# Kernel tuning notes

Measured on AMD Instinct MI355X. Metric: run time of the kernel, lower is better.

The kernel has to match this reference:

```python
import jax, jax.numpy as jnp
import numpy as np

B, N, L, H, N_NODE, STEP = 1024, 64, 64, 128, 50000, 2


def setup_inputs() -> dict:
    key = jax.random.key(0)
    ks = jax.random.split(key, 24)
    stdv = 1.0 / np.sqrt(H)
    u = lambda k, shape: jax.random.uniform(k, shape, jnp.float32, -stdv, stdv)
    emb = u(ks[0], (N_NODE + 1, H))
    emb = emb.at[0].set(0.0)  # padding_idx=0
    return {
        "A": jax.random.uniform(ks[1], (B, N, 2 * N), jnp.float32),
        "items": jax.random.randint(ks[2], (B, N), 0, N_NODE + 1, jnp.int32),
        "mask": jnp.ones((B, L), jnp.int32),
        "alias_input": jax.random.randint(ks[3], (B, L), 0, N, jnp.int32),
        "emb": emb,
        "w_in": u(ks[4], (H, H)), "b_in": u(ks[5], (H,)),
        "w_out": u(ks[6], (H, H)), "b_out": u(ks[7], (H,)),
        "b_iah": u(ks[8], (H,)), "b_oah": u(ks[9], (H,)),
        "wi": u(ks[10], (3 * H, 2 * H)), "bi": u(ks[11], (3 * H,)),
        "wh": u(ks[12], (3 * H, H)), "bh": u(ks[13], (3 * H,)),
        "w1": u(ks[14], (H, H)), "b1": u(ks[15], (H,)),
        "w2": u(ks[16], (H, H)), "b2": u(ks[17], (H,)),
        "wq": u(ks[18], (1, H)),
        "w3": u(ks[19], (H, 2 * H)), "b3": u(ks[20], (2 * H,))[:H],
    }


def _gru_cell(A, hidden, p):
    n = A.shape[1]
    h_in = hidden @ p["w_in"].T + p["b_in"]
    h_out = hidden @ p["w_out"].T + p["b_out"]
    input_in = jnp.einsum("bnm,bmh->bnh", A[:, :, :n], h_in) + p["b_iah"]
    input_out = jnp.einsum("bnm,bmh->bnh", A[:, :, n:], h_out) + p["b_oah"]
    input_emb = jnp.concatenate([input_in, input_out], axis=2)  # [B,N,2H]
    gi = input_emb @ p["wi"].T + p["bi"]
    gh = hidden @ p["wh"].T + p["bh"]
    i_r, i_i, i_n = jnp.split(gi, 3, axis=2)
    h_r, h_i, h_n = jnp.split(gh, 3, axis=2)
    update_gate = jax.nn.sigmoid(i_i + h_i)
    reset_gate = jax.nn.sigmoid(i_r + h_r)
    new_gate = jnp.tanh(reset_gate * h_n + i_n)
    return (1.0 - update_gate) * hidden + update_gate * new_gate


def reference(A, items, mask, alias_input, emb, w_in, b_in, w_out, b_out,
              b_iah, b_oah, wi, bi, wh, bh, w1, b1, w2, b2, wq, w3, b3):
    p = dict(w_in=w_in, b_in=b_in, w_out=w_out, b_out=b_out, b_iah=b_iah,
             b_oah=b_oah, wi=wi, bi=bi, wh=wh, bh=bh)
    hidden = emb[items]  # [B,N,H]
    for _ in range(STEP):
        hidden = _gru_cell(A, hidden, p)
    # gather session order: seq_hidden[b, l] = hidden[b, alias_input[b, l]]
    seq_hidden = jnp.take_along_axis(hidden, alias_input[:, :, None], axis=1)  # [B,L,H]
    last = jnp.sum(mask, axis=1) - 1  # [B]
    local_emb = jnp.take_along_axis(seq_hidden, last[:, None, None], axis=1)[:, 0]  # [B,H]
    q1 = (local_emb @ w1.T + b1)[:, None, :]
    q2 = seq_hidden @ w2.T + b2
    alpha = jax.nn.sigmoid(q1 + q2) @ wq.T  # [B,L,1]
    global_emb = jnp.sum(alpha * seq_hidden * mask[:, :, None].astype(seq_hidden.dtype), axis=1)
    return jnp.concatenate([local_emb, global_emb], axis=1) @ w3.T + b3
```

## Files before the change

kernel.cpp:

```cpp
#include <hip/hip_runtime.h>
#include <stdint.h>


#define BDIM 256
#define NB   1024
#define NN   64
#define HH   128
#define SH_STR 136
#define SX_STR 264

#define OFS_WIN  0
#define OFS_WOUT 16384
#define OFS_WI   32768
#define OFS_WH   131072
#define OFS_W2   180224
#define N_FRAGS  24576

typedef short v8s __attribute__((ext_vector_type(8)));
typedef float v4f __attribute__((ext_vector_type(4)));

__device__ __forceinline__ float b2f_lo(uint32_t u){
  union { uint32_t u; float f; } v; v.u = u << 16; return v.f;
}
__device__ __forceinline__ float b2f_hi(uint32_t u){
  union { uint32_t u; float f; } v; v.u = u & 0xffff0000u; return v.f;
}
__device__ __forceinline__ uint16_t f2b(float f){
  union { float f; uint32_t u; } v; v.f = f;
  uint32_t r = v.u + 0x7fffu + ((v.u >> 16) & 1u);
  return (uint16_t)(r >> 16);
}
__device__ __forceinline__ float b2f(uint16_t s){
  union { uint32_t u; float f; } v; v.u = ((uint32_t)s) << 16; return v.f;
}
__device__ __forceinline__ float sig_f(float x){ return 1.0f / (1.0f + __expf(-x)); }
__device__ __forceinline__ float tanh_f(float x){ return 1.0f - 2.0f / (__expf(2.0f*x) + 1.0f); }

__device__ __forceinline__ uint32_t pack2bf(float a, float b){
  union { float f; uint32_t u; } ua, ub; ua.f = a; ub.f = b;
  return __builtin_amdgcn_perm(ub.u + 0x8000u, ua.u + 0x8000u, 0x07060302u);
}

__device__ __forceinline__ v8s pack8(const float* __restrict__ p){
  float4 f0 = *reinterpret_cast<const float4*>(p);
  float4 f1 = *reinterpret_cast<const float4*>(p + 4);
  union { uint32_t u[4]; v8s v; } o;
  o.u[0] = pack2bf(f0.x, f0.y);
  o.u[1] = pack2bf(f0.z, f0.w);
  o.u[2] = pack2bf(f1.x, f1.y);
  o.u[3] = pack2bf(f1.z, f1.w);
  return o.v;
}

__device__ __forceinline__ v8s ldsA(const uint16_t* buf, int stride,
                                    int row_base, int k_base, int r, int q){
  return *reinterpret_cast<const v8s*>(&buf[(row_base + r) * stride + k_base + q * 8]);
}

__device__ __forceinline__ v8s ldfrag(const uint16_t* __restrict__ ws,
                                      int base, int tile, int lane){
  return *reinterpret_cast<const v8s*>(ws + base + (((size_t)tile * 64 + lane) << 3));
}

#define MFMA(a, b, c) __builtin_amdgcn_mfma_f32_16x16x32_bf16((a), (b), (c), 0, 0, 0)

__global__ __launch_bounds__(256) void pack_weights(
    const float* __restrict__ w_in, const float* __restrict__ w_out,
    const float* __restrict__ wi,   const float* __restrict__ wh,
    const float* __restrict__ w2,   uint16_t* __restrict__ ws)
{
  int gid = blockIdx.x * blockDim.x + threadIdx.x;
  if (gid >= N_FRAGS) return;
  const float* W; int C; int fi; int base;
  if (gid < 2048)       { W = w_in;  C = 128; fi = gid;         base = OFS_WIN; }
  else if (gid < 4096)  { W = w_out; C = 128; fi = gid - 2048;  base = OFS_WOUT; }
  else if (gid < 16384) { W = wi;    C = 256; fi = gid - 4096;  base = OFS_WI; }
  else if (gid < 22528) { W = wh;    C = 128; fi = gid - 16384; base = OFS_WH; }
  else                  { W = w2;    C = 128; fi = gid - 22528; base = OFS_W2; }
  int lane = fi & 63;
  int tile = fi >> 6;
  int tc   = C >> 5;
  int tr   = tile / tc, kc = tile - tr * tc;
  int r = lane & 15, q = lane >> 4;
  const float* p = W + (size_t)(tr * 16 + r) * C + kc * 32 + q * 8;
  *reinterpret_cast<v8s*>(ws + base + ((size_t)fi << 3)) = pack8(p);
}

__global__ __launch_bounds__(BDIM, 3) void srgnn_kernel(
    const float* __restrict__ A,
    const int*   __restrict__ items,
    const int*   __restrict__ mask,
    const int*   __restrict__ alias_input,
    const float* __restrict__ emb,
    const float* __restrict__ b_in,  const float* __restrict__ b_out,
    const float* __restrict__ b_iah, const float* __restrict__ b_oah,
    const float* __restrict__ bi,    const float* __restrict__ bh,
    const float* __restrict__ w1,    const float* __restrict__ b1,
    const float* __restrict__ b2,
    const float* __restrict__ wq,
    const float* __restrict__ w3,    const float* __restrict__ b3,
    const uint16_t* __restrict__ ws,
    float* __restrict__ out)
{
  __shared__ __align__(16) uint16_t sH[NN * SH_STR];
  __shared__ __align__(16) uint16_t sX[NN * SX_STR];
  __shared__ float sQ1[128], sGlob[128], sAPart[4][64], sAlpha[64];
  __shared__ int   sAliasRow[64], sMaskArr[64];

  const int t    = threadIdx.x;
  const int b    = blockIdx.x;
  const int lane = t & 63;
  const int wv   = __builtin_amdgcn_readfirstlane(t >> 6);
  const int r    = lane & 15;
  const int q    = lane >> 4;

  {
    const int* itb = items + b * NN;
    for (int j = t; j < NN * HH; j += BDIM) {
      int n = j >> 7, k = j & 127;
      sH[n * SH_STR + k] = f2b(emb[(size_t)itb[n] * HH + k]);
    }
    if (t < 64) {
      sAliasRow[t] = alias_input[b * 64 + t];
      sMaskArr[t]  = mask[b * 64 + t];
    }
  }

  v8s a2[4][2];
  {
    const int half = wv >> 1;
    #pragma unroll
    for (int mt = 0; mt < 4; ++mt)
      #pragma unroll
      for (int kk = 0; kk < 2; ++kk)
        a2[mt][kk] = pack8(A + (size_t)(b * NN + mt * 16 + r) * (2 * NN)
                             + half * 64 + kk * 32 + q * 8);
  }
  __syncthreads();

  for (int step = 0; step < 2; ++step) {
    {
      v8s a[4][4];
      #pragma unroll
      for (int mt = 0; mt < 4; ++mt)
        #pragma unroll
        for (int kk = 0; kk < 4; ++kk)
          a[mt][kk] = ldsA(sH, SH_STR, mt * 16, kk * 32, r, q);

      const int    wbase = (wv < 2) ? OFS_WIN : OFS_WOUT;
      const float* bsel  = (wv < 2) ? b_in : b_out;
      const int    ntofs = (wv < 2) ? 0 : 8;
      #pragma unroll 2
      for (int i = 0; i < 4; ++i) {
        int nt = wv * 4 + i;
        int tr = nt - ntofs;
        int c  = nt * 16 + r;
        float bini = bsel[tr * 16 + r];
        v4f acc0 = {bini, bini, bini, bini}, acc1 = acc0, acc2 = acc0, acc3 = acc0;
        #pragma unroll
        for (int kk = 0; kk < 4; ++kk) {
          v8s bf = ldfrag(ws, wbase, tr * 4 + kk, lane);
          acc0 = MFMA(a[0][kk], bf, acc0);
          acc1 = MFMA(a[1][kk], bf, acc1);
          acc2 = MFMA(a[2][kk], bf, acc2);
          acc3 = MFMA(a[3][kk], bf, acc3);
        }
        #pragma unroll
        for (int reg = 0; reg < 4; ++reg) {
          sX[(0  + q * 4 + reg) * SX_STR + c] = f2b(acc0[reg]);
          sX[(16 + q * 4 + reg) * SX_STR + c] = f2b(acc1[reg]);
          sX[(32 + q * 4 + reg) * SX_STR + c] = f2b(acc2[reg]);
          sX[(48 + q * 4 + reg) * SX_STR + c] = f2b(acc3[reg]);
        }
      }
    }

    {
      const float* bsel2 = (wv < 2) ? b_iah : b_oah;
      const int    wofs2 = (wv < 2) ? 0 : 128;
      #pragma unroll 1
      for (int i = 0; i < 4; ++i) {
        int nt = wv * 4 + i;
        int c  = nt * 16 + r;
        v8s b0, b1f;
        #pragma unroll
        for (int j = 0; j < 8; ++j) {
          b0[j]  = (short)sX[(q * 8 + j) * SX_STR + c];
          b1f[j] = (short)sX[(32 + q * 8 + j) * SX_STR + c];
        }
        float bini = bsel2[c - wofs2];
        v4f acc0 = {bini, bini, bini, bini}, acc1 = acc0, acc2 = acc0, acc3 = acc0;
        acc0 = MFMA(a2[0][0], b0, acc0); acc0 = MFMA(a2[0][1], b1f, acc0);
        acc1 = MFMA(a2[1][0], b0, acc1); acc1 = MFMA(a2[1][1], b1f, acc1);
        acc2 = MFMA(a2[2][0], b0, acc2); acc2 = MFMA(a2[2][1], b1f, acc2);
        acc3 = MFMA(a2[3][0], b0, acc3); acc3 = MFMA(a2[3][1], b1f, acc3);
        #pragma unroll
        for (int reg = 0; reg < 4; ++reg) {
          sX[(0  + q * 4 + reg) * SX_STR + c] = f2b(acc0[reg]);
          sX[(16 + q * 4 + reg) * SX_STR + c] = f2b(acc1[reg]);
          sX[(32 + q * 4 + reg) * SX_STR + c] = f2b(acc2[reg]);
          sX[(48 + q * 4 + reg) * SX_STR + c] = f2b(acc3[reg]);
        }
      }
    }
    __syncthreads();

    {
      const int h0 = wv * 32;
      uint32_t nhpk[2][8];

      #pragma unroll 1
      for (int u = 0; u < 2; ++u) {
        int h = h0 + u * 16 + r;
        float vR  = bi[h] + bh[h];
        float vI  = bi[128 + h] + bh[128 + h];
        float vNi = bi[256 + h];
        float vNh = bh[256 + h];
        v4f aR[4], aI[4], aNi[4], aNh[4];
        #pragma unroll
        for (int mt = 0; mt < 4; ++mt) {
          aR[mt]  = (v4f){vR, vR, vR, vR};
          aI[mt]  = (v4f){vI, vI, vI, vI};
          aNi[mt] = (v4f){vNi, vNi, vNi, vNi};
          aNh[mt] = (v4f){vNh, vNh, vNh, vNh};
        }
        const int trb = wv * 2 + u;
        #pragma unroll 2
        for (int kk = 0; kk < 8; ++kk) {
          v8s af0 = ldsA(sX, SX_STR, 0,  kk * 32, r, q);
          v8s af1 = ldsA(sX, SX_STR, 16, kk * 32, r, q);
          v8s af2 = ldsA(sX, SX_STR, 32, kk * 32, r, q);
          v8s af3 = ldsA(sX, SX_STR, 48, kk * 32, r, q);
          v8s bR = ldfrag(ws, OFS_WI, (0 * 8 + trb) * 8 + kk, lane);
          v8s bI = ldfrag(ws, OFS_WI, (8 + trb) * 8 + kk, lane);
          v8s bN = ldfrag(ws, OFS_WI, (16 + trb) * 8 + kk, lane);
          aR[0]  = MFMA(af0, bR, aR[0]);  aR[1]  = MFMA(af1, bR, aR[1]);
          aR[2]  = MFMA(af2, bR, aR[2]);  aR[3]  = MFMA(af3, bR, aR[3]);
          aI[0]  = MFMA(af0, bI, aI[0]);  aI[1]  = MFMA(af1, bI, aI[1]);
          aI[2]  = MFMA(af2, bI, aI[2]);  aI[3]  = MFMA(af3, bI, aI[3]);
          aNi[0] = MFMA(af0, bN, aNi[0]); aNi[1] = MFMA(af1, bN, aNi[1]);
          aNi[2] = MFMA(af2, bN, aNi[2]); aNi[3] = MFMA(af3, bN, aNi[3]);
        }
        #pragma unroll 2
        for (int kk = 0; kk < 4; ++kk) {
          v8s af0 = ldsA(sH, SH_STR, 0,  kk * 32, r, q);
          v8s af1 = ldsA(sH, SH_STR, 16, kk * 32, r, q);
          v8s af2 = ldsA(sH, SH_STR, 32, kk * 32, r, q);
          v8s af3 = ldsA(sH, SH_STR, 48, kk * 32, r, q);
          v8s bR = ldfrag(ws, OFS_WH, (0 * 8 + trb) * 4 + kk, lane);
          v8s bI = ldfrag(ws, OFS_WH, (8 + trb) * 4 + kk, lane);
          v8s bN = ldfrag(ws, OFS_WH, (16 + trb) * 4 + kk, lane);
          aR[0]  = MFMA(af0, bR, aR[0]);  aR[1]  = MFMA(af1, bR, aR[1]);
          aR[2]  = MFMA(af2, bR, aR[2]);  aR[3]  = MFMA(af3, bR, aR[3]);
          aI[0]  = MFMA(af0, bI, aI[0]);  aI[1]  = MFMA(af1, bI, aI[1]);
          aI[2]  = MFMA(af2, bI, aI[2]);  aI[3]  = MFMA(af3, bI, aI[3]);
          aNh[0] = MFMA(af0, bN, aNh[0]); aNh[1] = MFMA(af1, bN, aNh[1]);
          aNh[2] = MFMA(af2, bN, aNh[2]); aNh[3] = MFMA(af3, bN, aNh[3]);
        }
        #pragma unroll
        for (int mt = 0; mt < 4; ++mt) {
          #pragma unroll
          for (int rp = 0; rp < 2; ++rp) {
            uint32_t pk = 0;
            #pragma unroll
            for (int e = 0; e < 2; ++e) {
              int reg = rp * 2 + e;
              int row = mt * 16 + q * 4 + reg;
              float z  = sig_f(aI[mt][reg]);
              float rr = sig_f(aR[mt][reg]);
              float gg = tanh_f(fmaf(rr, aNh[mt][reg], aNi[mt][reg]));
              float hp = b2f(sH[row * SH_STR + h]);
              pk |= (uint32_t)f2b(fmaf(z, gg - hp, hp)) << (16 * e);
            }
            nhpk[u][mt * 2 + rp] = pk;
          }
        }
      }
      __syncthreads();

      #pragma unroll
      for (int u = 0; u < 2; ++u) {
        int h = h0 + u * 16 + r;
        #pragma unroll
        for (int mt = 0; mt < 4; ++mt)
          #pragma unroll
          for (int rp = 0; rp < 2; ++rp) {
            uint32_t pk = nhpk[u][mt * 2 + rp];
            int row = mt * 16 + q * 4 + rp * 2;
            sH[row * SH_STR + h]       = (uint16_t)(pk & 0xffff);
            sH[(row + 1) * SH_STR + h] = (uint16_t)(pk >> 16);
          }
      }
    }
    __syncthreads();
  }

  int msum = 0;
  #pragma unroll
  for (int l = 0; l < 64; ++l) msum += sMaskArr[l];
  const int lastRow = sAliasRow[msum - 1];

  if (t < HH) {
    const float4* w14 = reinterpret_cast<const float4*>(w1 + (size_t)t * HH);
    const uint2*  lr  = reinterpret_cast<const uint2*>(&sH[lastRow * SH_STR]);
    float a0 = b1[t], a1 = 0.f, a2v = 0.f, a3 = 0.f;
    #pragma unroll 8
    for (int j = 0; j < 32; ++j) {
      float4 w = w14[j]; uint2 v = lr[j];
      a0  = fmaf(b2f_lo(v.x), w.x, a0);  a1 = fmaf(b2f_hi(v.x), w.y, a1);
      a2v = fmaf(b2f_lo(v.y), w.z, a2v); a3 = fmaf(b2f_hi(v.y), w.w, a3);
    }
    sQ1[t] = (a0 + a1) + (a2v + a3);
  }
  __syncthreads();

  {
    v8s a[4][4];
    #pragma unroll
    for (int mt = 0; mt < 4; ++mt) {
      int row = sAliasRow[mt * 16 + r];
      #pragma unroll
      for (int kk = 0; kk < 4; ++kk)
        a[mt][kk] = *reinterpret_cast<const v8s*>(&sH[row * SH_STR + kk * 32 + q * 8]);
    }
    float part[16];
    #pragma unroll
    for (int i = 0; i < 16; ++i) part[i] = 0.f;
    #pragma unroll
    for (int u = 0; u < 2; ++u) {
      int h = wv * 32 + u * 16 + r;
      float binit = sQ1[h] + b2[h];
      v4f acc[4];
      #pragma unroll
      for (int mt = 0; mt < 4; ++mt) acc[mt] = (v4f){binit, binit, binit, binit};
      #pragma unroll
      for (int kk = 0; kk < 4; ++kk) {
        v8s bf = ldfrag(ws, OFS_W2, (wv * 2 + u) * 4 + kk, lane);
        acc[0] = MFMA(a[0][kk], bf, acc[0]);
        acc[1] = MFMA(a[1][kk], bf, acc[1]);
        acc[2] = MFMA(a[2][kk], bf, acc[2]);
        acc[3] = MFMA(a[3][kk], bf, acc[3]);
      }
      float wqh = wq[h];
      #pragma unroll
      for (int mt = 0; mt < 4; ++mt)
        #pragma unroll
        for (int reg = 0; reg < 4; ++reg)
          part[mt * 4 + reg] += sig_f(acc[mt][reg]) * wqh;
    }
    #pragma unroll
    for (int m = 1; m <= 8; m <<= 1)
      #pragma unroll
      for (int i = 0; i < 16; ++i)
        part[i] += __shfl_xor(part[i], m);
    if (r == 0) {
      #pragma unroll
      for (int mt = 0; mt < 4; ++mt)
        #pragma unroll
        for (int reg = 0; reg < 4; ++reg)
          sAPart[wv][mt * 16 + q * 4 + reg] = part[mt * 4 + reg];
    }
  }
  __syncthreads();
  if (t < 64) {
    sAlpha[t] = (sAPart[0][t] + sAPart[1][t] + sAPart[2][t] + sAPart[3][t])
              * (float)sMaskArr[t];
  }
  __syncthreads();
  if (t < HH) {
    float acc = 0.0f;
    #pragma unroll
    for (int l = 0; l < 64; ++l)
      acc = fmaf(sAlpha[l], b2f(sH[sAliasRow[l] * SH_STR + t]), acc);
    sGlob[t] = acc;
  }
  __syncthreads();
  if (t < HH) {
    const float4* w34 = reinterpret_cast<const float4*>(w3 + (size_t)t * 256);
    const uint2*  lr  = reinterpret_cast<const uint2*>(&sH[lastRow * SH_STR]);
    float a0 = b3[t], a1 = 0.f, a2v = 0.f, a3 = 0.f;
    #pragma unroll 8
    for (int j = 0; j < 32; ++j) {
      float4 w = w34[j]; uint2 v = lr[j];
      a0  = fmaf(b2f_lo(v.x), w.x, a0);  a1 = fmaf(b2f_hi(v.x), w.y, a1);
      a2v = fmaf(b2f_lo(v.y), w.z, a2v); a3 = fmaf(b2f_hi(v.y), w.w, a3);
    }
    const float4* w34b = w34 + 32;
    #pragma unroll 8
    for (int j = 0; j < 32; ++j) {
      float4 w = w34b[j];
      a0  = fmaf(sGlob[4*j+0], w.x, a0);  a1 = fmaf(sGlob[4*j+1], w.y, a1);
      a2v = fmaf(sGlob[4*j+2], w.z, a2v); a3 = fmaf(sGlob[4*j+3], w.w, a3);
    }
    out[b * HH + t] = (a0 + a1) + (a2v + a3);
  }
}

extern "C" void kernel_launch(void* const* d_in, const int* in_sizes, int n_in,
                              void* d_out, int out_size, void* d_ws, size_t ws_size,
                              hipStream_t stream) {
  const float* A          = (const float*)d_in[0];
  const int*   items      = (const int*)  d_in[1];
  const int*   mask       = (const int*)  d_in[2];
  const int*   alias_in   = (const int*)  d_in[3];
  const float* emb        = (const float*)d_in[4];
  const float* w_in       = (const float*)d_in[5];
  const float* b_in       = (const float*)d_in[6];
  const float* w_out      = (const float*)d_in[7];
  const float* b_out      = (const float*)d_in[8];
  const float* b_iah      = (const float*)d_in[9];
  const float* b_oah      = (const float*)d_in[10];
  const float* wi         = (const float*)d_in[11];
  const float* bi         = (const float*)d_in[12];
  const float* wh         = (const float*)d_in[13];
  const float* bh         = (const float*)d_in[14];
  const float* w1         = (const float*)d_in[15];
  const float* b1         = (const float*)d_in[16];
  const float* w2         = (const float*)d_in[17];
  const float* b2         = (const float*)d_in[18];
  const float* wq         = (const float*)d_in[19];
  const float* w3         = (const float*)d_in[20];
  const float* b3         = (const float*)d_in[21];
  float* out = (float*)d_out;
  uint16_t* wsp = (uint16_t*)d_ws;

  hipLaunchKernelGGL(pack_weights, dim3((N_FRAGS + 255) / 256), dim3(256), 0, stream,
                     w_in, w_out, wi, wh, w2, wsp);
  hipLaunchKernelGGL(srgnn_kernel, dim3(NB), dim3(BDIM), 0, stream,
                     A, items, mask, alias_in, emb,
                     b_in, b_out, b_iah, b_oah, bi, bh,
                     w1, b1, b2, wq, w3, b3, wsp, out);
}
```

Before: 257.5 us.

## Interleave GRU input/hidden MFMA loops, prefetch weight fragments, split epilogue across all threads

```diff
diff --git a/kernel.cpp b/kernel.cpp
--- a/kernel.cpp
+++ b/kernel.cpp
@@ -104,8 +104,14 @@
 {
   __shared__ __align__(16) uint16_t sH[NN * SH_STR];
   __shared__ __align__(16) uint16_t sX[NN * SX_STR];
-  __shared__ float sQ1[128], sGlob[128], sAPart[4][64], sAlpha[64];
-  __shared__ int   sAliasRow[64], sMaskArr[64];
+  __shared__ int sAliasRow[64], sMaskArr[64];
+
+  float* sF      = reinterpret_cast<float*>(sX);
+  float* sQ1v    = sF;
+  float* sGlobv  = sF + 128;
+  float* sAPartv = sF + 256;
+  float* sAlphav = sF + 512;
+  float* sP      = sF + 576;
 
   const int t    = threadIdx.x;
   const int b    = blockIdx.x;
@@ -203,6 +209,15 @@
         }
       }
     }
+
+    v8s pR[2], pI[2], pN[2];
+    #pragma unroll
+    for (int u = 0; u < 2; ++u) {
+      int trb = wv * 2 + u;
+      pR[u] = ldfrag(ws, OFS_WI, (0  + trb) * 8, lane);
+      pI[u] = ldfrag(ws, OFS_WI, (8  + trb) * 8, lane);
+      pN[u] = ldfrag(ws, OFS_WI, (16 + trb) * 8, lane);
+    }
     __syncthreads();
 
     {
@@ -225,37 +240,51 @@
           aNh[mt] = (v4f){vNh, vNh, vNh, vNh};
         }
         const int trb = wv * 2 + u;
-        #pragma unroll 2
-        for (int kk = 0; kk < 8; ++kk) {
+
+        #pragma unroll 1
+        for (int kk = 0; kk < 4; ++kk) {
+          v8s bR = (kk == 0) ? pR[u] : ldfrag(ws, OFS_WI, (0  + trb) * 8 + kk, lane);
+          v8s bI = (kk == 0) ? pI[u] : ldfrag(ws, OFS_WI, (8  + trb) * 8 + kk, lane);
+          v8s bN = (kk == 0) ? pN[u] : ldfrag(ws, OFS_WI, (16 + trb) * 8 + kk, lane);
+          v8s cR = ldfrag(ws, OFS_WH, (0  + trb) * 4 + kk, lane);
+          v8s cI = ldfrag(ws, OFS_WH, (8  + trb) * 4 + kk, lane);
+          v8s cN = ldfrag(ws, OFS_WH, (16 + trb) * 4 + kk, lane);
           v8s af0 = ldsA(sX, SX_STR, 0,  kk * 32, r, q);
           v8s af1 = ldsA(sX, SX_STR, 16, kk * 32, r, q);
           v8s af2 = ldsA(sX, SX_STR, 32, kk * 32, r, q);
           v8s af3 = ldsA(sX, SX_STR, 48, kk * 32, r, q);
-          v8s bR = ldfrag(ws, OFS_WI, (0 * 8 + trb) * 8 + kk, lane);
-          v8s bI = ldfrag(ws, OFS_WI, (8 + trb) * 8 + kk, lane);
-          v8s bN = ldfrag(ws, OFS_WI, (16 + trb) * 8 + kk, lane);
+          v8s ag0 = ldsA(sH, SH_STR, 0,  kk * 32, r, q);
+          v8s ag1 = ldsA(sH, SH_STR, 16, kk * 32, r, q);
+          v8s ag2 = ldsA(sH, SH_STR, 32, kk * 32, r, q);
+          v8s ag3 = ldsA(sH, SH_STR, 48, kk * 32, r, q);
           aR[0]  = MFMA(af0, bR, aR[0]);  aR[1]  = MFMA(af1, bR, aR[1]);
           aR[2]  = MFMA(af2, bR, aR[2]);  aR[3]  = MFMA(af3, bR, aR[3]);
           aI[0]  = MFMA(af0, bI, aI[0]);  aI[1]  = MFMA(af1, bI, aI[1]);
           aI[2]  = MFMA(af2, bI, aI[2]);  aI[3]  = MFMA(af3, bI, aI[3]);
           aNi[0] = MFMA(af0, bN, aNi[0]); aNi[1] = MFMA(af1, bN, aNi[1]);
           aNi[2] = MFMA(af2, bN, aNi[2]); aNi[3] = MFMA(af3, bN, aNi[3]);
+          aR[0]  = MFMA(ag0, cR, aR[0]);  aR[1]  = MFMA(ag1, cR, aR[1]);
+          aR[2]  = MFMA(ag2, cR, aR[2]);  aR[3]  = MFMA(ag3, cR, aR[3]);
+          aI[0]  = MFMA(ag0, cI, aI[0]);  aI[1]  = MFMA(ag1, cI, aI[1]);
+          aI[2]  = MFMA(ag2, cI, aI[2]);  aI[3]  = MFMA(ag3, cI, aI[3]);
+          aNh[0] = MFMA(ag0, cN, aNh[0]); aNh[1] = MFMA(ag1, cN, aNh[1]);
+          aNh[2] = MFMA(ag2, cN, aNh[2]); aNh[3] = MFMA(ag3, cN, aNh[3]);
         }
         #pragma unroll 2
-        for (int kk = 0; kk < 4; ++kk) {
-          v8s af0 = ldsA(sH, SH_STR, 0,  kk * 32, r, q);
-          v8s af1 = ldsA(sH, SH_STR, 16, kk * 32, r, q);
-          v8s af2 = ldsA(sH, SH_STR, 32, kk * 32, r, q);
-          v8s af3 = ldsA(sH, SH_STR, 48, kk * 32, r, q);
-          v8s bR = ldfrag(ws, OFS_WH, (0 * 8 + trb) * 4 + kk, lane);
-          v8s bI = ldfrag(ws, OFS_WH, (8 + trb) * 4 + kk, lane);
-          v8s bN = ldfrag(ws, OFS_WH, (16 + trb) * 4 + kk, lane);
+        for (int kk = 4; kk < 8; ++kk) {
+          v8s bR = ldfrag(ws, OFS_WI, (0  + trb) * 8 + kk, lane);
+          v8s bI = ldfrag(ws, OFS_WI, (8  + trb) * 8 + kk, lane);
+          v8s bN = ldfrag(ws, OFS_WI, (16 + trb) * 8 + kk, lane);
+          v8s af0 = ldsA(sX, SX_STR, 0,  kk * 32, r, q);
+          v8s af1 = ldsA(sX, SX_STR, 16, kk * 32, r, q);
+          v8s af2 = ldsA(sX, SX_STR, 32, kk * 32, r, q);
+          v8s af3 = ldsA(sX, SX_STR, 48, kk * 32, r, q);
           aR[0]  = MFMA(af0, bR, aR[0]);  aR[1]  = MFMA(af1, bR, aR[1]);
           aR[2]  = MFMA(af2, bR, aR[2]);  aR[3]  = MFMA(af3, bR, aR[3]);
           aI[0]  = MFMA(af0, bI, aI[0]);  aI[1]  = MFMA(af1, bI, aI[1]);
           aI[2]  = MFMA(af2, bI, aI[2]);  aI[3]  = MFMA(af3, bI, aI[3]);
-          aNh[0] = MFMA(af0, bN, aNh[0]); aNh[1] = MFMA(af1, bN, aNh[1]);
-          aNh[2] = MFMA(af2, bN, aNh[2]); aNh[3] = MFMA(af3, bN, aNh[3]);
+          aNi[0] = MFMA(af0, bN, aNi[0]); aNi[1] = MFMA(af1, bN, aNi[1]);
+          aNi[2] = MFMA(af2, bN, aNi[2]); aNi[3] = MFMA(af3, bN, aNi[3]);
         }
         #pragma unroll
         for (int mt = 0; mt < 4; ++mt) {
@@ -299,19 +328,23 @@
   #pragma unroll
   for (int l = 0; l < 64; ++l) msum += sMaskArr[l];
   const int lastRow = sAliasRow[msum - 1];
-
-  if (t < HH) {
-    const float4* w14 = reinterpret_cast<const float4*>(w1 + (size_t)t * HH);
-    const uint2*  lr  = reinterpret_cast<const uint2*>(&sH[lastRow * SH_STR]);
-    float a0 = b1[t], a1 = 0.f, a2v = 0.f, a3 = 0.f;
+  const int hh  = t & 127;
+  const int seg = t >> 7;
+
+  {
+    const float4* w14 = reinterpret_cast<const float4*>(w1 + (size_t)hh * HH + seg * 64);
+    const uint2*  lr  = reinterpret_cast<const uint2*>(&sH[lastRow * SH_STR + seg * 64]);
+    float a0 = seg ? 0.f : b1[hh], a1 = 0.f, a2v = 0.f, a3 = 0.f;
     #pragma unroll 8
-    for (int j = 0; j < 32; ++j) {
+    for (int j = 0; j < 16; ++j) {
       float4 w = w14[j]; uint2 v = lr[j];
       a0  = fmaf(b2f_lo(v.x), w.x, a0);  a1 = fmaf(b2f_hi(v.x), w.y, a1);
       a2v = fmaf(b2f_lo(v.y), w.z, a2v); a3 = fmaf(b2f_hi(v.y), w.w, a3);
     }
-    sQ1[t] = (a0 + a1) + (a2v + a3);
-  }
+    sP[seg * 128 + hh] = (a0 + a1) + (a2v + a3);
+  }
+  __syncthreads();
+  if (t < HH) sQ1v[t] = sP[t] + sP[128 + t];
   __syncthreads();
 
   {
@@ -329,7 +362,7 @@
     #pragma unroll
     for (int u = 0; u < 2; ++u) {
       int h = wv * 32 + u * 16 + r;
-      float binit = sQ1[h] + b2[h];
+      float binit = sQ1v[h] + b2[h];
       v4f acc[4];
       #pragma unroll
       for (int mt = 0; mt < 4; ++mt) acc[mt] = (v4f){binit, binit, binit, binit};
@@ -358,42 +391,52 @@
       for (int mt = 0; mt < 4; ++mt)
         #pragma unroll
         for (int reg = 0; reg < 4; ++reg)
-          sAPart[wv][mt * 16 + q * 4 + reg] = part[mt * 4 + reg];
+          sAPartv[wv * 64 + mt * 16 + q * 4 + reg] = part[mt * 4 + reg];
     }
   }
   __syncthreads();
   if (t < 64) {
-    sAlpha[t] = (sAPart[0][t] + sAPart[1][t] + sAPart[2][t] + sAPart[3][t])
-              * (float)sMaskArr[t];
-  }
-  __syncthreads();
-  if (t < HH) {
+    sAlphav[t] = (sAPartv[t] + sAPartv[64 + t] + sAPartv[128 + t] + sAPartv[192 + t])
+               * (float)sMaskArr[t];
+  }
+  __syncthreads();
+
+  {
     float acc = 0.0f;
     #pragma unroll
-    for (int l = 0; l < 64; ++l)
-      acc = fmaf(sAlpha[l], b2f(sH[sAliasRow[l] * SH_STR + t]), acc);
-    sGlob[t] = acc;
-  }
-  __syncthreads();
-  if (t < HH) {
-    const float4* w34 = reinterpret_cast<const float4*>(w3 + (size_t)t * 256);
-    const uint2*  lr  = reinterpret_cast<const uint2*>(&sH[lastRow * SH_STR]);
-    float a0 = b3[t], a1 = 0.f, a2v = 0.f, a3 = 0.f;
-    #pragma unroll 8
-    for (int j = 0; j < 32; ++j) {
-      float4 w = w34[j]; uint2 v = lr[j];
-      a0  = fmaf(b2f_lo(v.x), w.x, a0);  a1 = fmaf(b2f_hi(v.x), w.y, a1);
-      a2v = fmaf(b2f_lo(v.y), w.z, a2v); a3 = fmaf(b2f_hi(v.y), w.w, a3);
-    }
-    const float4* w34b = w34 + 32;
-    #pragma unroll 8
-    for (int j = 0; j < 32; ++j) {
-      float4 w = w34b[j];
-      a0  = fmaf(sGlob[4*j+0], w.x, a0);  a1 = fmaf(sGlob[4*j+1], w.y, a1);
-      a2v = fmaf(sGlob[4*j+2], w.z, a2v); a3 = fmaf(sGlob[4*j+3], w.w, a3);
-    }
-    out[b * HH + t] = (a0 + a1) + (a2v + a3);
-  }
+    for (int l = 0; l < 32; ++l) {
+      int ll = seg * 32 + l;
+      acc = fmaf(sAlphav[ll], b2f(sH[sAliasRow[ll] * SH_STR + hh]), acc);
+    }
+    sP[seg * 128 + hh] = acc;
+  }
+  __syncthreads();
+  if (t < HH) sGlobv[t] = sP[t] + sP[128 + t];
+  __syncthreads();
+
+  {
+    const float4* w34 = reinterpret_cast<const float4*>(w3 + (size_t)hh * 256 + seg * 128);
+    float a0 = seg ? 0.f : b3[hh], a1 = 0.f, a2v = 0.f, a3 = 0.f;
+    if (seg == 0) {
+      const uint2* lr = reinterpret_cast<const uint2*>(&sH[lastRow * SH_STR]);
+      #pragma unroll 8
+      for (int j = 0; j < 32; ++j) {
+        float4 w = w34[j]; uint2 v = lr[j];
+        a0  = fmaf(b2f_lo(v.x), w.x, a0);  a1 = fmaf(b2f_hi(v.x), w.y, a1);
+        a2v = fmaf(b2f_lo(v.y), w.z, a2v); a3 = fmaf(b2f_hi(v.y), w.w, a3);
+      }
+    } else {
+      #pragma unroll 8
+      for (int j = 0; j < 32; ++j) {
+        float4 w = w34[j];
+        a0  = fmaf(sGlobv[4*j+0], w.x, a0);  a1 = fmaf(sGlobv[4*j+1], w.y, a1);
+        a2v = fmaf(sGlobv[4*j+2], w.z, a2v); a3 = fmaf(sGlobv[4*j+3], w.w, a3);
+      }
+    }
+    sP[seg * 128 + hh] = (a0 + a1) + (a2v + a3);
+  }
+  __syncthreads();
+  if (t < HH) out[b * HH + t] = sP[t] + sP[128 + t];
 }
 
 extern "C" void kernel_launch(void* const* d_in, const int* in_sizes, int n_in,
```

Measured after the change: 285.2 us. 10.8% more time.
